# Kernel tuning notes

Measured on AMD Instinct MI355X. Metric: run time of the kernel, lower is better.

## Reference

```python
import jax, jax.numpy as jnp
import numpy as np

B = 65536
IN = 512
HID = 512
NQ = 8
NGATES = 4  # input, forget, output, cell


def setup_inputs() -> dict:
    key = jax.random.key(0)
    ks = jax.random.split(key, 7)
    fan1 = IN + HID
    return {
        "x": jax.random.normal(ks[0], (B, IN), dtype=jnp.float32),
        "h": jax.random.normal(ks[1], (B, HID), dtype=jnp.float32),
        "c": jax.random.normal(ks[2], (B, HID), dtype=jnp.float32),
        # stacked params for the 4 gate networks (PyTorch Linear layout: [out, in])
        "W1": jax.random.normal(ks[3], (NGATES, NQ, fan1), dtype=jnp.float32) / np.sqrt(fan1).astype(np.float32),
        "b1": jax.random.normal(ks[4], (NGATES, NQ), dtype=jnp.float32) * 0.01,
        "W2": jax.random.normal(ks[5], (NGATES, HID, NQ), dtype=jnp.float32) / np.sqrt(NQ).astype(np.float32),
        "b2": jax.random.normal(ks[6], (NGATES, HID), dtype=jnp.float32) * 0.01,
    }


def reference(x, h, c, W1, b1, W2, b2):
    # combined: [B, IN+HID]
    combined = jnp.concatenate([x, h], axis=-1)
    # batched first layer over the 4 gates: [B, 4, NQ]
    z = jnp.tanh(jnp.einsum("bi,gqi->bgq", combined, W1) + b1)
    # batched second layer: [B, 4, HID], sigmoid on ALL gates (incl. cell gate, per source)
    gates = jax.nn.sigmoid(jnp.einsum("bgq,ghq->bgh", z, W2) + b2)
    i, f, o, g = gates[:, 0], gates[:, 1], gates[:, 2], gates[:, 3]
    c_new = f * c + i * g
    h_new = o * jnp.tanh(c_new)
    return h_new, c_new
```

## Files before the change

### kernel.cpp

```cpp
#include <hip/hip_runtime.h>
#include <math.h>

#define B_TOTAL 65536
#define IN_DIM 512
#define HID_DIM 512
#define FAN1 1024
#define NQ 8
#define NGATES 4

__global__ __launch_bounds__(256, 4)
void k1_gemv(const float* __restrict__ x, const float* __restrict__ h,
             const float* __restrict__ W1, const float* __restrict__ b1,
             float* __restrict__ Z) {
    __shared__ __align__(16) float tile[64][64];

    const int tid     = threadIdx.x;
    const int lane    = tid & 63;
    const int g       = __builtin_amdgcn_readfirstlane(tid >> 6);
    const int rowbase = blockIdx.x * 64;

    float acc[8];
#pragma unroll
    for (int j = 0; j < 8; ++j) acc[j] = 0.0f;

    for (int kc = 0; kc < FAN1; kc += 64) {
        const float* src = (kc < IN_DIM) ? (x + kc) : (h + (kc - IN_DIM));

        __syncthreads();
#pragma unroll
        for (int i = 0; i < 4; ++i) {
            int idx = tid + 256 * i;
            int r   = idx >> 4;
            int kg  = idx & 15;
            float4 v = *(const float4*)(src + (size_t)(rowbase + r) * 512 + kg * 4);
            *(float4*)&tile[r][(kg ^ (r & 7)) << 2] = v;
        }
        __syncthreads();

#pragma unroll 2
        for (int kg = 0; kg < 16; ++kg) {
            float4 cv = *(const float4*)&tile[lane][(kg ^ (lane & 7)) << 2];
#pragma unroll
            for (int j = 0; j < 8; ++j) {
                float4 wv = *(const float4*)(W1 + (size_t)(g * 8 + j) * FAN1 + kc + kg * 4);
                acc[j] = fmaf(cv.x, wv.x, acc[j]);
                acc[j] = fmaf(cv.y, wv.y, acc[j]);
                acc[j] = fmaf(cv.z, wv.z, acc[j]);
                acc[j] = fmaf(cv.w, wv.w, acc[j]);
            }
        }
    }

    float o[8];
#pragma unroll
    for (int j = 0; j < 8; ++j) {
        o[j] = tanhf(acc[j] + b1[g * 8 + j]);
    }
    float* zp = Z + (size_t)(rowbase + lane) * 32 + g * 8;
    *(float4*)(zp + 0) = make_float4(o[0], o[1], o[2], o[3]);
    *(float4*)(zp + 4) = make_float4(o[4], o[5], o[6], o[7]);
}

__device__ __forceinline__ float sigmoid_f(float v) {
    return 1.0f / (1.0f + __expf(-v));
}
__device__ __forceinline__ float tanh_fast(float v) {
    return 1.0f - 2.0f / (__expf(2.0f * v) + 1.0f);
}

__global__ __launch_bounds__(256, 4)
void k2_gates(const float* __restrict__ Z, const float* __restrict__ c,
              const float* __restrict__ W2, const float* __restrict__ b2,
              float* __restrict__ out) {
    const int tid     = threadIdx.x;
    const int rowbase = blockIdx.x * 64;

    float w2r[2][4][8];
    float b2r[2][4];
#pragma unroll
    for (int hi = 0; hi < 2; ++hi) {
        int hh = tid + 256 * hi;
#pragma unroll
        for (int g = 0; g < 4; ++g) {
            const float* wp = W2 + (size_t)(g * HID_DIM + hh) * NQ;
            float4 a = *(const float4*)(wp + 0);
            float4 b = *(const float4*)(wp + 4);
            w2r[hi][g][0] = a.x; w2r[hi][g][1] = a.y;
            w2r[hi][g][2] = a.z; w2r[hi][g][3] = a.w;
            w2r[hi][g][4] = b.x; w2r[hi][g][5] = b.y;
            w2r[hi][g][6] = b.z; w2r[hi][g][7] = b.w;
            b2r[hi][g] = b2[g * HID_DIM + hh];
        }
    }

    const size_t c_off = (size_t)B_TOTAL * HID_DIM;

    for (int r = 0; r < 64; ++r) {
        const int row = rowbase + r;
        const float* zrow = Z + (size_t)row * 32;
        float zz[32];
#pragma unroll
        for (int t = 0; t < 8; ++t) {
            float4 zv = *(const float4*)(zrow + 4 * t);
            zz[4 * t + 0] = zv.x; zz[4 * t + 1] = zv.y;
            zz[4 * t + 2] = zv.z; zz[4 * t + 3] = zv.w;
        }
#pragma unroll
        for (int hi = 0; hi < 2; ++hi) {
            int hh = tid + 256 * hi;
            float cv = c[(size_t)row * HID_DIM + hh];
            float pre[4];
#pragma unroll
            for (int g = 0; g < 4; ++g) {
                float a = b2r[hi][g];
#pragma unroll
                for (int q = 0; q < 8; ++q)
                    a = fmaf(zz[g * 8 + q], w2r[hi][g][q], a);
                pre[g] = a;
            }
            float ig = sigmoid_f(pre[0]);
            float fg = sigmoid_f(pre[1]);
            float og = sigmoid_f(pre[2]);
            float gg = sigmoid_f(pre[3]);
            float cn = fg * cv + ig * gg;
            float hn = og * tanh_fast(cn);
            out[(size_t)row * HID_DIM + hh]         = hn;
            out[c_off + (size_t)row * HID_DIM + hh] = cn;
        }
    }
}

extern "C" void kernel_launch(void* const* d_in, const int* in_sizes, int n_in,
                              void* d_out, int out_size, void* d_ws, size_t ws_size,
                              hipStream_t stream) {
    const float* x  = (const float*)d_in[0];
    const float* h  = (const float*)d_in[1];
    const float* c  = (const float*)d_in[2];
    const float* W1 = (const float*)d_in[3];
    const float* b1 = (const float*)d_in[4];
    const float* W2 = (const float*)d_in[5];
    const float* b2 = (const float*)d_in[6];
    float* out = (float*)d_out;
    float* Z   = (float*)d_ws;

    hipLaunchKernelGGL(k1_gemv, dim3(B_TOTAL / 64), dim3(256), 0, stream,
                       x, h, W1, b1, Z);
    hipLaunchKernelGGL(k2_gates, dim3(B_TOTAL / 64), dim3(256), 0, stream,
                       Z, c, W2, b2, out);
}
```

Before: 648.3 us.

## Fuse GEMV and gate kernels into one kernel with shared-memory Z

Merges the first-layer GEMV and the gate/cell-update kernels into a single kernel. The tanh outputs are kept in shared memory instead of being written to a global workspace and read back, and a second launch is removed. Each thread now handles two adjacent hidden units with float2 loads and stores of c and the outputs. Hardware reciprocal and a fast tanh replace exact division and tanhf, which lowers accuracy slightly and raises register pressure from holding 64 W2 weights per thread.

```diff
diff --git a/kernel.cpp b/kernel.cpp
--- a/kernel.cpp
+++ b/kernel.cpp
@@ -8,11 +8,24 @@
 #define NQ 8
 #define NGATES 4
 
+__device__ __forceinline__ float fast_rcp(float x) {
+    return __builtin_amdgcn_rcpf(x);
+}
+__device__ __forceinline__ float sigmoid_f(float v) {
+    return fast_rcp(1.0f + __expf(-v));
+}
+__device__ __forceinline__ float tanh_fast(float v) {
+    return 1.0f - 2.0f * fast_rcp(__expf(2.0f * v) + 1.0f);
+}
+
 __global__ __launch_bounds__(256, 4)
-void k1_gemv(const float* __restrict__ x, const float* __restrict__ h,
-             const float* __restrict__ W1, const float* __restrict__ b1,
-             float* __restrict__ Z) {
+void fused_qlstm(const float* __restrict__ x, const float* __restrict__ h,
+                 const float* __restrict__ c,
+                 const float* __restrict__ W1, const float* __restrict__ b1,
+                 const float* __restrict__ W2, const float* __restrict__ b2,
+                 float* __restrict__ out) {
     __shared__ __align__(16) float tile[64][64];
+    __shared__ __align__(16) float zsh[64][36];
 
     const int tid     = threadIdx.x;
     const int lane    = tid & 63;
@@ -51,82 +64,69 @@
         }
     }
 
-    float o[8];
+    {
+        float o[8];
 #pragma unroll
-    for (int j = 0; j < 8; ++j) {
-        o[j] = tanhf(acc[j] + b1[g * 8 + j]);
+        for (int j = 0; j < 8; ++j)
+            o[j] = tanh_fast(acc[j] + b1[g * 8 + j]);
+        *(float4*)&zsh[lane][g * 8 + 0] = make_float4(o[0], o[1], o[2], o[3]);
+        *(float4*)&zsh[lane][g * 8 + 4] = make_float4(o[4], o[5], o[6], o[7]);
     }
-    float* zp = Z + (size_t)(rowbase + lane) * 32 + g * 8;
-    *(float4*)(zp + 0) = make_float4(o[0], o[1], o[2], o[3]);
-    *(float4*)(zp + 4) = make_float4(o[4], o[5], o[6], o[7]);
-}
 
-__device__ __forceinline__ float sigmoid_f(float v) {
-    return 1.0f / (1.0f + __expf(-v));
-}
-__device__ __forceinline__ float tanh_fast(float v) {
-    return 1.0f - 2.0f / (__expf(2.0f * v) + 1.0f);
-}
+    float  w2r[4][16];
+    float2 b2r[4];
+#pragma unroll
+    for (int gg = 0; gg < 4; ++gg) {
+        const float* wp = W2 + ((size_t)gg * HID_DIM + 2 * tid) * NQ;
+        float4 a = *(const float4*)(wp + 0);
+        float4 b = *(const float4*)(wp + 4);
+        float4 cc = *(const float4*)(wp + 8);
+        float4 d = *(const float4*)(wp + 12);
+        w2r[gg][0]  = a.x;  w2r[gg][1]  = a.y;  w2r[gg][2]  = a.z;  w2r[gg][3]  = a.w;
+        w2r[gg][4]  = b.x;  w2r[gg][5]  = b.y;  w2r[gg][6]  = b.z;  w2r[gg][7]  = b.w;
+        w2r[gg][8]  = cc.x; w2r[gg][9]  = cc.y; w2r[gg][10] = cc.z; w2r[gg][11] = cc.w;
+        w2r[gg][12] = d.x;  w2r[gg][13] = d.y;  w2r[gg][14] = d.z;  w2r[gg][15] = d.w;
+        b2r[gg] = *(const float2*)(b2 + gg * HID_DIM + 2 * tid);
+    }
 
-__global__ __launch_bounds__(256, 4)
-void k2_gates(const float* __restrict__ Z, const float* __restrict__ c,
-              const float* __restrict__ W2, const float* __restrict__ b2,
-              float* __restrict__ out) {
-    const int tid     = threadIdx.x;
-    const int rowbase = blockIdx.x * 64;
-
-    float w2r[2][4][8];
-    float b2r[2][4];
-#pragma unroll
-    for (int hi = 0; hi < 2; ++hi) {
-        int hh = tid + 256 * hi;
-#pragma unroll
-        for (int g = 0; g < 4; ++g) {
-            const float* wp = W2 + (size_t)(g * HID_DIM + hh) * NQ;
-            float4 a = *(const float4*)(wp + 0);
-            float4 b = *(const float4*)(wp + 4);
-            w2r[hi][g][0] = a.x; w2r[hi][g][1] = a.y;
-            w2r[hi][g][2] = a.z; w2r[hi][g][3] = a.w;
-            w2r[hi][g][4] = b.x; w2r[hi][g][5] = b.y;
-            w2r[hi][g][6] = b.z; w2r[hi][g][7] = b.w;
-            b2r[hi][g] = b2[g * HID_DIM + hh];
-        }
-    }
+    __syncthreads();
 
     const size_t c_off = (size_t)B_TOTAL * HID_DIM;
 
     for (int r = 0; r < 64; ++r) {
         const int row = rowbase + r;
-        const float* zrow = Z + (size_t)row * 32;
-        float zz[32];
+        float2 cv = *(const float2*)(c + (size_t)row * HID_DIM + 2 * tid);
+
+        float pre0[4], pre1[4];
 #pragma unroll
-        for (int t = 0; t < 8; ++t) {
-            float4 zv = *(const float4*)(zrow + 4 * t);
-            zz[4 * t + 0] = zv.x; zz[4 * t + 1] = zv.y;
-            zz[4 * t + 2] = zv.z; zz[4 * t + 3] = zv.w;
+        for (int gg = 0; gg < 4; ++gg) {
+            float4 za = *(const float4*)&zsh[r][gg * 8 + 0];
+            float4 zb = *(const float4*)&zsh[r][gg * 8 + 4];
+            float p0 = b2r[gg].x, p1 = b2r[gg].y;
+            p0 = fmaf(za.x, w2r[gg][0], p0);  p1 = fmaf(za.x, w2r[gg][8],  p1);
+            p0 = fmaf(za.y, w2r[gg][1], p0);  p1 = fmaf(za.y, w2r[gg][9],  p1);
+            p0 = fmaf(za.z, w2r[gg][2], p0);  p1 = fmaf(za.z, w2r[gg][10], p1);
+            p0 = fmaf(za.w, w2r[gg][3], p0);  p1 = fmaf(za.w, w2r[gg][11], p1);
+            p0 = fmaf(zb.x, w2r[gg][4], p0);  p1 = fmaf(zb.x, w2r[gg][12], p1);
+            p0 = fmaf(zb.y, w2r[gg][5], p0);  p1 = fmaf(zb.y, w2r[gg][13], p1);
+            p0 = fmaf(zb.z, w2r[gg][6], p0);  p1 = fmaf(zb.z, w2r[gg][14], p1);
+            p0 = fmaf(zb.w, w2r[gg][7], p0);  p1 = fmaf(zb.w, w2r[gg][15], p1);
+            pre0[gg] = p0;
+            pre1[gg] = p1;
         }
-#pragma unroll
-        for (int hi = 0; hi < 2; ++hi) {
-            int hh = tid + 256 * hi;
-            float cv = c[(size_t)row * HID_DIM + hh];
-            float pre[4];
-#pragma unroll
-            for (int g = 0; g < 4; ++g) {
-                float a = b2r[hi][g];
-#pragma unroll
-                for (int q = 0; q < 8; ++q)
-                    a = fmaf(zz[g * 8 + q], w2r[hi][g][q], a);
-                pre[g] = a;
-            }
-            float ig = sigmoid_f(pre[0]);
-            float fg = sigmoid_f(pre[1]);
-            float og = sigmoid_f(pre[2]);
-            float gg = sigmoid_f(pre[3]);
-            float cn = fg * cv + ig * gg;
-            float hn = og * tanh_fast(cn);
-            out[(size_t)row * HID_DIM + hh]         = hn;
-            out[c_off + (size_t)row * HID_DIM + hh] = cn;
-        }
+
+        float i0 = sigmoid_f(pre0[0]), i1 = sigmoid_f(pre1[0]);
+        float f0 = sigmoid_f(pre0[1]), f1 = sigmoid_f(pre1[1]);
+        float o0 = sigmoid_f(pre0[2]), o1 = sigmoid_f(pre1[2]);
+        float g0 = sigmoid_f(pre0[3]), g1 = sigmoid_f(pre1[3]);
+
+        float cn0 = f0 * cv.x + i0 * g0;
+        float cn1 = f1 * cv.y + i1 * g1;
+        float hn0 = o0 * tanh_fast(cn0);
+        float hn1 = o1 * tanh_fast(cn1);
+
+        *(float2*)(out + (size_t)row * HID_DIM + 2 * tid)         = make_float2(hn0, hn1);
+        *(float2*)(out + c_off + (size_t)row * HID_DIM + 2 * tid) = make_float2(cn0, cn1);
     }
 }
 
@@ -141,10 +141,7 @@
     const float* W2 = (const float*)d_in[5];
     const float* b2 = (const float*)d_in[6];
     float* out = (float*)d_out;
-    float* Z   = (float*)d_ws;
 
-    hipLaunchKernelGGL(k1_gemv, dim3(B_TOTAL / 64), dim3(256), 0, stream,
-                       x, h, W1, b1, Z);
-    hipLaunchKernelGGL(k2_gates, dim3(B_TOTAL / 64), dim3(256), 0, stream,
-                       Z, c, W2, b2, out);
+    hipLaunchKernelGGL(fused_qlstm, dim3(B_TOTAL / 64), dim3(256), 0, stream,
+                       x, h, c, W1, b1, W2, b2, out);
 }
```

Result: no change. 658.9 us (+1.6%).
